# Kernel tuning notes

Hardware: AMD Instinct MI355X
Metric: run time of the kernel (lower is better)

Reference implementation:

```python
import jax, jax.numpy as jnp
import numpy as np

B, T, HW, N, HID, K, OUT = 8, 64, 64, 64, 64, 2, 1
DT = 0.1


def setup_inputs() -> dict:
    key = jax.random.key(0)
    ks = jax.random.split(key, 16)
    nrm = lambda k, shape, s: jax.random.normal(k, shape, jnp.float32) * s
    return {
        "frames": jax.random.uniform(ks[0], (B, T, HW, HW, 3), jnp.float32),
        "adjacency": jax.random.uniform(ks[1], (B, T, N, N), jnp.float32) / N,
        "hidden0": jnp.zeros((B, N, HID), jnp.float32),
        "Wc1": nrm(ks[2], (32, 3, 3, 3), 0.3), "bc1": jnp.zeros(32, jnp.float32),
        "Wc2": nrm(ks[3], (64, 32, 3, 3), 0.08), "bc2": jnp.zeros(64, jnp.float32),
        "Wc3": nrm(ks[4], (128, 64, 3, 3), 0.06), "bc3": jnp.zeros(128, jnp.float32),
        "We": nrm(ks[5], (128, HID), 0.09), "be": jnp.zeros(HID, jnp.float32),
        "Wh": nrm(ks[6], (K + 1, HID, HID), 0.12),
        "Wx": nrm(ks[7], (K + 1, HID, HID), 0.12),
        "bg": jnp.zeros(HID, jnp.float32),
        "tau": jnp.ones(HID, jnp.float32),
        "Ap": nrm(ks[8], (HID,), 1.0),
        "Wd1": nrm(ks[9], (HID, 128), 0.12), "bd1": jnp.zeros(128, jnp.float32),
        "Wd2": nrm(ks[10], (128, 64), 0.09), "bd2": jnp.zeros(64, jnp.float32),
        "Wd3": nrm(ks[11], (64, OUT), 0.12), "bd3": jnp.zeros(OUT, jnp.float32),
    }


def _conv_relu(x, w, b, stride):
    # torch Conv2d(k=3, stride=2, padding=1) == explicit padding (1,1)
    y = jax.lax.conv_general_dilated(
        x, w, (stride, stride), [(1, 1), (1, 1)],
        dimension_numbers=("NCHW", "OIHW", "NCHW"))
    return jax.nn.relu(y + b[None, :, None, None])


def _forward(frames, adjacency, hidden0, Wc1, bc1, Wc2, bc2, Wc3, bc3,
             We, be, Wh, Wx, bg, tau, Ap, Wd1, bd1, Wd2, bd2, Wd3, bd3):
    Bn, Tn, Hh, Ww, C = frames.shape
    # faithful to torch .view(-1, C, H, W): raw memory reinterpretation
    x = frames.reshape(Bn * Tn, C, Hh, Ww)
    x = _conv_relu(x, Wc1, bc1, 2)   # [BT,32,32,32]
    x = _conv_relu(x, Wc2, bc2, 2)   # [BT,64,16,16]
    x = _conv_relu(x, Wc3, bc3, 2)   # [BT,128,8,8]; AdaptiveAvgPool2d((8,8)) is identity here
    feats = x.reshape(Bn, Tn, 128, 8, 8).transpose(0, 1, 3, 4, 2).reshape(Bn, Tn, 64, 128)
    node = feats @ We + be           # [B,T,N,HID]

    Kp = Wh.shape[0] - 1
    eye = jnp.eye(adjacency.shape[-1], dtype=frames.dtype)

    def step(h, inputs):
        xt, At = inputs              # [B,N,HID], [B,N,N]
        powers = [jnp.broadcast_to(eye, At.shape)]
        p = At
        for _ in range(Kp):          # static K-loop -> [I, A, ..., A^K]
            powers.append(p)
            p = jnp.matmul(p, At)
        S = jnp.stack(powers)        # [K+1,B,N,N]
        z = jnp.einsum("bnd,kde->kbne", h, Wh) + jnp.einsum("bnd,kde->kbne", xt, Wx)
        gc = jnp.einsum("kbnm,kbme->bne", S, z) + bg
        f = jnp.tanh(gc)
        h_next = h + DT * (-(1.0 / tau + f) * h + f * Ap)  # liquid time-constant Euler step
        m = h_next.mean(axis=1)      # [B,HID]
        d = jax.nn.relu(m @ Wd1 + bd1)
        d = jax.nn.relu(d @ Wd2 + bd2)
        c = d @ Wd3 + bd3            # [B,OUT]
        return h_next, c

    xs = (node.transpose(1, 0, 2, 3), adjacency.transpose(1, 0, 2, 3))
    final_h, controls = jax.lax.scan(step, hidden0, xs)
    controls = controls.transpose(1, 0, 2)  # [B,T,OUT]
    return controls, final_h


def reference(frames, adjacency, hidden0, Wc1, bc1, Wc2, bc2, Wc3, bc3,
              We, be, Wh, Wx, bg, tau, Ap, Wd1, bd1, Wd2, bd2, Wd3, bd3):
    return _forward(frames, adjacency, hidden0, Wc1, bc1, Wc2, bc2, Wc3, bc3,
                    We, be, Wh, Wx, bg, tau, Ap, Wd1, bd1, Wd2, bd2, Wd3, bd3)
```

## Files before the change

kernel.cpp:

```cpp
#include <hip/hip_runtime.h>
#include <hip/hip_bf16.h>

#define SH 68
#define DT_C 0.1f

typedef short bfrag __attribute__((ext_vector_type(8)));
typedef _Float16 hfrag __attribute__((ext_vector_type(8)));
typedef float f32x4 __attribute__((ext_vector_type(4)));

union FU { bfrag v; unsigned short s[8]; uint4 q; };
union HU { hfrag v; unsigned short s[8]; uint4 q; };

__device__ __forceinline__ unsigned short bf16_rn(float x) {
  union { float f; unsigned u; } v; v.f = x;
  unsigned r = v.u + 0x7fffu + ((v.u >> 16) & 1u);
  return (unsigned short)(r >> 16);
}
__device__ __forceinline__ float bf16_tof(unsigned short h) {
  union { unsigned u; float f; } v; v.u = ((unsigned)h) << 16; return v.f;
}
__device__ __forceinline__ unsigned short bfu(float x) {
  union { __hip_bfloat16 b; unsigned short u; } cv;
  cv.b = __float2bfloat16(x);
  return cv.u;
}
__device__ __forceinline__ float tanh_f(float x) {
  return 1.0f - 2.0f / (__expf(2.0f * x) + 1.0f);
}
__device__ __forceinline__ void h16split(float v, unsigned short& hu, unsigned short& lu) {
  union { _Float16 h; unsigned short u; } a, b;
  a.h = (_Float16)v;
  b.h = (_Float16)(v - (float)a.h);
  hu = a.u; lu = b.u;
}
__device__ __forceinline__ unsigned short h16hi(float v) {
  union { _Float16 h; unsigned short u; } a; a.h = (_Float16)v; return a.u;
}

__device__ __forceinline__ void mm16(const float* __restrict__ A,
                                     const float* __restrict__ B, int sb,
                                     float acc[4][4], int n0, int e0) {
  #pragma unroll 4
  for (int k4 = 0; k4 < 16; ++k4) {
    float4 av0 = *(const float4*)(A + (n0+0)*SH + k4*4);
    float4 av1 = *(const float4*)(A + (n0+1)*SH + k4*4);
    float4 av2 = *(const float4*)(A + (n0+2)*SH + k4*4);
    float4 av3 = *(const float4*)(A + (n0+3)*SH + k4*4);
    const float a0j[4] = {av0.x, av0.y, av0.z, av0.w};
    const float a1j[4] = {av1.x, av1.y, av1.z, av1.w};
    const float a2j[4] = {av2.x, av2.y, av2.z, av2.w};
    const float a3j[4] = {av3.x, av3.y, av3.z, av3.w};
    #pragma unroll
    for (int j = 0; j < 4; ++j) {
      const float4 bv = *(const float4*)(B + (k4*4+j)*sb + e0);
      acc[0][0]+=a0j[j]*bv.x; acc[0][1]+=a0j[j]*bv.y; acc[0][2]+=a0j[j]*bv.z; acc[0][3]+=a0j[j]*bv.w;
      acc[1][0]+=a1j[j]*bv.x; acc[1][1]+=a1j[j]*bv.y; acc[1][2]+=a1j[j]*bv.z; acc[1][3]+=a1j[j]*bv.w;
      acc[2][0]+=a2j[j]*bv.x; acc[2][1]+=a2j[j]*bv.y; acc[2][2]+=a2j[j]*bv.z; acc[2][3]+=a2j[j]*bv.w;
      acc[3][0]+=a3j[j]*bv.x; acc[3][1]+=a3j[j]*bv.y; acc[3][2]+=a3j[j]*bv.z; acc[3][3]+=a3j[j]*bv.w;
    }
  }
}

__global__ __launch_bounds__(256) void wprep_k(const float* __restrict__ Wc2,
                                               const float* __restrict__ Wc3,
                                               const float* __restrict__ Wh,
                                               unsigned short* __restrict__ W2h,
                                               unsigned short* __restrict__ W2l,
                                               unsigned short* __restrict__ W3h,
                                               unsigned short* __restrict__ W3l,
                                               unsigned short* __restrict__ WTh,
                                               unsigned short* __restrict__ WTl) {
  int i = blockIdx.x * 256 + threadIdx.x;
  if (i < 18432) {
    int oc = i / 288, rem = i % 288, pos = rem >> 5, ic = rem & 31;
    float v = Wc2[oc*288 + ic*9 + pos];
    h16split(v, W2h[i], W2l[i]);
  } else if (i < 18432 + 73728) {
    int j = i - 18432;
    int oc = j / 576, rem = j % 576, pos = rem >> 6, ic = rem & 63;
    float v = Wc3[oc*576 + ic*9 + pos];
    h16split(v, W3h[j], W3l[j]);
  } else if (i < 18432 + 73728 + 12288) {
    int j = i - 92160;
    int k3 = j >> 12, rem = j & 4095, din = rem >> 6, dout = rem & 63;
    float v = Wh[j];
    unsigned short hi = bf16_rn(v);
    WTh[k3*4096 + dout*64 + din] = hi;
    WTl[k3*4096 + dout*64 + din] = bf16_rn(v - bf16_tof(hi));
  }
}

__global__ __launch_bounds__(256) void conv1_k(const float* __restrict__ frames,
                                               const float* __restrict__ W,
                                               const float* __restrict__ bias,
                                               unsigned short* __restrict__ c1h) {
  __shared__ __align__(16) float sIn[12288];
  int bt = blockIdx.x, tid = threadIdx.x;
  const float4* src = (const float4*)(frames + (size_t)bt * 12288);
  for (int i = tid; i < 3072; i += 256) ((float4*)sIn)[i] = src[i];
  __syncthreads();
  for (int p = tid; p < 1024; p += 256) {
    int ho = p >> 5, wo = p & 31, hi0 = ho*2-1, wi0 = wo*2-1;
    int obase = (((ho*2 + (wo&1))*16 + (wo>>1)))*8;
    for (int ocb = 0; ocb < 4; ++ocb) {
      float acc[8];
      #pragma unroll
      for (int j = 0; j < 8; ++j) acc[j] = bias[ocb*8+j];
      for (int ic = 0; ic < 3; ++ic) {
        float win[9];
        #pragma unroll
        for (int kh = 0; kh < 3; ++kh) {
          int hi = hi0 + kh;
          #pragma unroll
          for (int kw = 0; kw < 3; ++kw) {
            int wi = wi0 + kw;
            win[kh*3+kw] = (hi>=0 && hi<64 && wi>=0 && wi<64) ? sIn[ic*4096 + hi*64 + wi] : 0.f;
          }
        }
        #pragma unroll
        for (int j = 0; j < 8; ++j) {
          const float* wp = W + (size_t)(ocb*8+j)*27 + ic*9;
          #pragma unroll
          for (int k = 0; k < 9; ++k) acc[j] += win[k] * wp[k];
        }
      }
      ushort hh[8];
      #pragma unroll
      for (int j = 0; j < 8; ++j) hh[j] = h16hi(fmaxf(acc[j], 0.f));
      *(uint4*)&c1h[(size_t)bt*32768 + ocb*8192 + obase] = *(uint4*)hh;
    }
  }
}

#define MFMAH(a, bb, cc) __builtin_amdgcn_mfma_f32_16x16x32_f16((a), (bb), (cc), 0, 0, 0)

__global__ __launch_bounds__(256) void conv2m_k(const unsigned short* __restrict__ c1h,
                                                const unsigned short* __restrict__ W2h,
                                                const unsigned short* __restrict__ W2l,
                                                const float* __restrict__ bias,
                                                unsigned short* __restrict__ c2h) {
  __shared__ __align__(16) unsigned short sH[32768];
  int bt = blockIdx.x, tid = threadIdx.x;
  {
    const uint4* gh = (const uint4*)(c1h + (size_t)bt*32768);
    for (int i = tid; i < 4096; i += 256) ((uint4*)sH)[i] = gh[i];
  }
  __syncthreads();
  int lane = tid & 63, w = tid >> 6, g = lane >> 4, c = lane & 15;
  f32x4 acc[4][4] = {};
  const uint4 z4 = make_uint4(0,0,0,0);
  #pragma unroll
  for (int pos = 0; pos < 9; ++pos) {
    const int kh = pos / 3, kw = pos % 3;
    HU Ah[4];
    #pragma unroll
    for (int m = 0; m < 4; ++m) {
      int pix = w*64 + m*16 + c;
      int ho = pix >> 4, wo = pix & 15;
      int hi = 2*ho - 1 + kh, wi = 2*wo - 1 + kw;
      bool ok = (hi >= 0) & (wi >= 0);
      int hic = ok ? hi : 0, wic = ok ? wi : 0;
      int a = (((g*32 + hic)*2 + (wic & 1))*16 + (wic >> 1))*8;
      uint4 vh = *(const uint4*)&sH[a];
      Ah[m].q = ok ? vh : z4;
    }
    HU Bh[4], Bl[4];
    #pragma unroll
    for (int n = 0; n < 4; ++n) {
      int off = (n*16 + c)*288 + pos*32 + g*8;
      Bh[n].q = *(const uint4*)(W2h + off);
      Bl[n].q = *(const uint4*)(W2l + off);
    }
    #pragma unroll
    for (int m = 0; m < 4; ++m)
      #pragma unroll
      for (int n = 0; n < 4; ++n) {
        acc[m][n] = MFMAH(Ah[m].v, Bh[n].v, acc[m][n]);
        acc[m][n] = MFMAH(Ah[m].v, Bl[n].v, acc[m][n]);
      }
  }
  #pragma unroll
  for (int n = 0; n < 4; ++n) {
    int oc = n*16 + c;
    float bv = bias[oc];
    int ks3 = oc >> 3, il = oc & 7;
    #pragma unroll
    for (int m = 0; m < 4; ++m) {
      #pragma unroll
      for (int r = 0; r < 4; ++r) {
        int pix = w*64 + m*16 + 4*g + r;
        int ho = pix >> 4, wo = pix & 15;
        float v = fmaxf(acc[m][n][r] + bv, 0.f);
        size_t dst = (size_t)bt*16384 + ((((ks3*16 + ho)*2 + (wo&1))*8 + (wo>>1)))*8 + il;
        c2h[dst] = h16hi(v);
      }
    }
  }
}

__global__ __launch_bounds__(256) void conv3m_k(const unsigned short* __restrict__ c2h,
                                                const unsigned short* __restrict__ W3h,
                                                const unsigned short* __restrict__ W3l,
                                                const float* __restrict__ bias,
                                                float* __restrict__ c3) {
  __shared__ __align__(16) unsigned short sH[16384];
  int bt = blockIdx.x, tid = threadIdx.x;
  {
    const uint4* gh = (const uint4*)(c2h + (size_t)bt*16384);
    for (int i = tid; i < 2048; i += 256) ((uint4*)sH)[i] = gh[i];
  }
  __syncthreads();
  int lane = tid & 63, w = tid >> 6, g = lane >> 4, c = lane & 15;
  f32x4 acc[8] = {};
  const uint4 z4 = make_uint4(0,0,0,0);
  int pix = w*16 + c;
  int ho = pix >> 3, wo = pix & 7;
  #pragma unroll
  for (int pos = 0; pos < 9; ++pos) {
    const int kh = pos / 3, kw = pos % 3;
    int hi = 2*ho - 1 + kh, wi = 2*wo - 1 + kw;
    bool ok = (hi >= 0) & (wi >= 0);
    int hic = ok ? hi : 0, wic = ok ? wi : 0;
    #pragma unroll
    for (int ih = 0; ih < 2; ++ih) {
      int icg = ih*4 + g;
      int a = ((((icg*16 + hic)*2 + (wic & 1))*8 + (wic >> 1)))*8;
      HU Ah;
      uint4 vh = *(const uint4*)&sH[a];
      Ah.q = ok ? vh : z4;
      #pragma unroll
      for (int n = 0; n < 8; ++n) {
        int off = (n*16 + c)*576 + pos*64 + ih*32 + g*8;
        HU Bh, Bl;
        Bh.q = *(const uint4*)(W3h + off);
        Bl.q = *(const uint4*)(W3l + off);
        acc[n] = MFMAH(Ah.v, Bh.v, acc[n]);
        acc[n] = MFMAH(Ah.v, Bl.v, acc[n]);
      }
    }
  }
  #pragma unroll
  for (int n = 0; n < 8; ++n) {
    int oc = n*16 + c;
    float bv = bias[oc];
    #pragma unroll
    for (int r = 0; r < 4; ++r) {
      int po = w*16 + 4*g + r;
      c3[(size_t)(bt*128 + oc)*64 + po] = fmaxf(acc[n][r] + bv, 0.f);
    }
  }
}

__global__ __launch_bounds__(256) void embed_k(const float* __restrict__ c3,
                                               const float* __restrict__ We,
                                               const float* __restrict__ be,
                                               float* __restrict__ node) {
  __shared__ float sF[64*133];
  __shared__ __align__(16) float sWe[8192];
  int bt = blockIdx.x, tid = threadIdx.x;
  const float* src = c3 + (size_t)bt * 8192;
  for (int i = tid; i < 8192; i += 256) sF[(i & 63)*133 + (i >> 6)] = src[i];
  const float4* w4 = (const float4*)We;
  for (int i = tid; i < 2048; i += 256) ((float4*)sWe)[i] = w4[i];
  __syncthreads();
  int lane = tid & 63, w = tid >> 6, nsub = lane >> 4, eb = lane & 15;
  int n0 = w*16 + nsub*4, e0 = eb*4;
  float acc[4][4];
  #pragma unroll
  for (int jj = 0; jj < 4; ++jj)
    #pragma unroll
    for (int ee = 0; ee < 4; ++ee) acc[jj][ee] = be[e0+ee];
  for (int c = 0; c < 128; ++c) {
    float a0 = sF[(n0+0)*133+c];
    float a1 = sF[(n0+1)*133+c];
    float a2 = sF[(n0+2)*133+c];
    float a3 = sF[(n0+3)*133+c];
    const float4 bv = *(const float4*)&sWe[c*64 + e0];
    acc[0][0]+=a0*bv.x; acc[0][1]+=a0*bv.y; acc[0][2]+=a0*bv.z; acc[0][3]+=a0*bv.w;
    acc[1][0]+=a1*bv.x; acc[1][1]+=a1*bv.y; acc[1][2]+=a1*bv.z; acc[1][3]+=a1*bv.w;
    acc[2][0]+=a2*bv.x; acc[2][1]+=a2*bv.y; acc[2][2]+=a2*bv.z; acc[2][3]+=a2*bv.w;
    acc[3][0]+=a3*bv.x; acc[3][1]+=a3*bv.y; acc[3][2]+=a3*bv.z; acc[3][3]+=a3*bv.w;
  }
  float4* nd = (float4*)(node + (size_t)bt * 4096);
  #pragma unroll
  for (int jj = 0; jj < 4; ++jj)
    nd[(n0+jj)*16 + eb] = make_float4(acc[jj][0], acc[jj][1], acc[jj][2], acc[jj][3]);
}

__global__ __launch_bounds__(256) void prep_k(const float* __restrict__ adj,
                                              const float* __restrict__ node,
                                              const float* __restrict__ Wx,
                                              unsigned short* __restrict__ Abf,
                                              unsigned short* __restrict__ A2bf,
                                              float* __restrict__ gxg) {
  __shared__ __align__(16) float sA[64*SH], sA2[64*SH], sN[64*SH], sZ[64*SH];
  int bt = blockIdx.x, tid = threadIdx.x;
  {
    const float4* a4 = (const float4*)(adj + (size_t)bt * 4096);
    const float4* n4 = (const float4*)(node + (size_t)bt * 4096);
    for (int i = tid; i < 1024; i += 256) {
      int r = i >> 4, c = (i & 15) * 4;
      *(float4*)&sA[r*SH+c] = a4[i];
      *(float4*)&sN[r*SH+c] = n4[i];
    }
  }
  __syncthreads();
  int lane = tid & 63, w = tid >> 6, nsub = lane >> 4, eb = lane & 15;
  int n0 = w*16 + nsub*4, e0 = eb*4;
  float4* gxout = (float4*)(gxg + (size_t)bt * 4096);
  for (int i = tid; i < 1024; i += 256) {
    int r = i >> 4, c0 = (i & 15) * 4;
    ushort4 o;
    o.x = bf16_rn(sA[r*SH+c0+0]); o.y = bf16_rn(sA[r*SH+c0+1]);
    o.z = bf16_rn(sA[r*SH+c0+2]); o.w = bf16_rn(sA[r*SH+c0+3]);
    *(ushort4*)&Abf[(size_t)bt*4096 + r*64 + c0] = o;
  }
  {
    float a2t[4][4] = {};
    mm16(sA, sA, SH, a2t, n0, e0);
    #pragma unroll
    for (int jj = 0; jj < 4; ++jj) {
      *(float4*)&sA2[(n0+jj)*SH+e0] = make_float4(a2t[jj][0], a2t[jj][1], a2t[jj][2], a2t[jj][3]);
      ushort4 o;
      o.x = bf16_rn(a2t[jj][0]); o.y = bf16_rn(a2t[jj][1]);
      o.z = bf16_rn(a2t[jj][2]); o.w = bf16_rn(a2t[jj][3]);
      *(ushort4*)&A2bf[(size_t)bt*4096 + (n0+jj)*64 + e0] = o;
    }
  }
  {
    float t[4][4] = {};
    mm16(sN, Wx + 4096, 64, t, n0, e0);
    #pragma unroll
    for (int jj = 0; jj < 4; ++jj)
      *(float4*)&sZ[(n0+jj)*SH+e0] = make_float4(t[jj][0], t[jj][1], t[jj][2], t[jj][3]);
  }
  __syncthreads();
  float gx[4][4] = {};
  mm16(sA, sZ, SH, gx, n0, e0);
  __syncthreads();
  {
    float t[4][4] = {};
    mm16(sN, Wx + 8192, 64, t, n0, e0);
    #pragma unroll
    for (int jj = 0; jj < 4; ++jj)
      *(float4*)&sZ[(n0+jj)*SH+e0] = make_float4(t[jj][0], t[jj][1], t[jj][2], t[jj][3]);
  }
  __syncthreads();
  mm16(sA2, sZ, SH, gx, n0, e0);
  mm16(sN, Wx, 64, gx, n0, e0);
  #pragma unroll
  for (int jj = 0; jj < 4; ++jj)
    gxout[(n0+jj)*16 + eb] = make_float4(gx[jj][0], gx[jj][1], gx[jj][2], gx[jj][3]);
}

#define MFMA(a, bb, cc) __builtin_amdgcn_mfma_f32_16x16x32_bf16((a), (bb), (cc), 0, 0, 0)

__global__ __launch_bounds__(1024, 4) void seq2_k(
    const unsigned short* __restrict__ Abf, const unsigned short* __restrict__ A2bf,
    const float* __restrict__ gxg, const float* __restrict__ h0,
    const unsigned short* __restrict__ WTh, const unsigned short* __restrict__ WTl,
    const float* __restrict__ bg, const float* __restrict__ tau, const float* __restrict__ Apv,
    float* __restrict__ mout, float* __restrict__ out) {
  __shared__ unsigned short sHh[64*72];
  __shared__ unsigned short sA[2][64*72], sA2[2][64*72];
  __shared__ unsigned short sZ1[64*72], sZ2[64*72];
  __shared__ float sPart[64*17];
  int b = blockIdx.x, tid = threadIdx.x;
  int lane = tid & 63, w = tid >> 6, g = lane >> 4, c = lane & 15;
  int mt = w & 3, nt = w >> 2;
  int e = nt*16 + c;
  int mrow = mt*16 + 4*g;
  float itau = 1.f/tau[e], apv = Apv[e], bgv = bg[e];
  FU wf[3][2][2];
  #pragma unroll
  for (int k3 = 0; k3 < 3; ++k3)
    #pragma unroll
    for (int kt = 0; kt < 2; ++kt) {
      int off = k3*4096 + e*64 + kt*32 + 8*g;
      wf[k3][kt][0].q = *(const uint4*)(WTh + off);
      wf[k3][kt][1].q = *(const uint4*)(WTl + off);
    }
  float hm[4];
  #pragma unroll
  for (int r = 0; r < 4; ++r) hm[r] = h0[(size_t)b*4096 + (mrow+r)*64 + e];
  #pragma unroll
  for (int r = 0; r < 4; ++r) sHh[(mrow+r)*72 + e] = bfu(hm[r]);
  {
    int row = tid >> 4, k0 = (tid & 15) * 4;
    *(uint2*)&sA[0][row*72 + k0]  = *(const uint2*)(Abf  + (size_t)b*64*4096 + tid*4);
    *(uint2*)&sA2[0][row*72 + k0] = *(const uint2*)(A2bf + (size_t)b*64*4096 + tid*4);
  }
  __syncthreads();
  #pragma unroll 1
  for (int t = 0; t < 64; ++t) {
    int cur = t & 1;
    size_t bt = (size_t)b*64 + t;
    int tn = (t < 63) ? t + 1 : t;
    uint2 pa  = *(const uint2*)(Abf  + ((size_t)b*64 + tn)*4096 + tid*4);
    uint2 pa2 = *(const uint2*)(A2bf + ((size_t)b*64 + tn)*4096 + tid*4);
    float gxv[4];
    {
      const float* gp = gxg + bt*4096;
      #pragma unroll
      for (int r = 0; r < 4; ++r) gxv[r] = gp[(mrow+r)*64 + e];
    }
    FU ha[2];
    #pragma unroll
    for (int kt = 0; kt < 2; ++kt)
      ha[kt].q = *(const uint4*)&sHh[(mt*16 + c)*72 + kt*32 + 8*g];
    f32x4 a1a = {0.f,0.f,0.f,0.f}, a1b = {0.f,0.f,0.f,0.f};
    f32x4 a2a = {0.f,0.f,0.f,0.f}, a2b = {0.f,0.f,0.f,0.f};
    a1a = MFMA(ha[0].v, wf[1][0][0].v, a1a);
    a1a = MFMA(ha[0].v, wf[1][0][1].v, a1a);
    a1b = MFMA(ha[1].v, wf[1][1][0].v, a1b);
    a1b = MFMA(ha[1].v, wf[1][1][1].v, a1b);
    a2a = MFMA(ha[0].v, wf[2][0][0].v, a2a);
    a2a = MFMA(ha[0].v, wf[2][0][1].v, a2a);
    a2b = MFMA(ha[1].v, wf[2][1][0].v, a2b);
    a2b = MFMA(ha[1].v, wf[2][1][1].v, a2b);
    f32x4 a1 = a1a + a1b, a2 = a2a + a2b;
    {
      ushort4 o1, o2;
      o1.x = bfu(a1[0]); o1.y = bfu(a1[1]); o1.z = bfu(a1[2]); o1.w = bfu(a1[3]);
      o2.x = bfu(a2[0]); o2.y = bfu(a2[1]); o2.z = bfu(a2[2]); o2.w = bfu(a2[3]);
      *(ushort4*)&sZ1[e*72 + mrow] = o1;
      *(ushort4*)&sZ2[e*72 + mrow] = o2;
    }
    __syncthreads();
    f32x4 acc0 = {0.f,0.f,0.f,0.f}, acc1 = {0.f,0.f,0.f,0.f};
    #pragma unroll
    for (int kt = 0; kt < 2; ++kt) {
      FU aA, aA2, z1f, z2f;
      int ao = (mt*16 + c)*72 + kt*32 + 8*g;
      aA.q  = *(const uint4*)&sA[cur][ao];
      aA2.q = *(const uint4*)&sA2[cur][ao];
      z1f.q = *(const uint4*)&sZ1[e*72 + kt*32 + 8*g];
      z2f.q = *(const uint4*)&sZ2[e*72 + kt*32 + 8*g];
      f32x4& acc = kt ? acc1 : acc0;
      acc = MFMA(ha[kt].v, wf[0][kt][0].v, acc);
      acc = MFMA(ha[kt].v, wf[0][kt][1].v, acc);
      acc = MFMA(aA.v,  z1f.v, acc);
      acc = MFMA(aA2.v, z2f.v, acc);
    }
    f32x4 acc = acc0 + acc1;
    float ps = 0.f;
    #pragma unroll
    for (int r = 0; r < 4; ++r) {
      float gc = acc[r] + gxv[r] + bgv;
      float f = tanh_f(gc);
      float hn = hm[r] + DT_C * (-(itau + f) * hm[r] + f * apv);
      hm[r] = hn;
      ps += hn;
      sHh[(mrow+r)*72 + e] = bfu(hn);
    }
    sPart[e*17 + mt*4 + g] = ps;
    {
      int row = tid >> 4, k0 = (tid & 15) * 4;
      *(uint2*)&sA[cur^1][row*72 + k0]  = pa;
      *(uint2*)&sA2[cur^1][row*72 + k0] = pa2;
    }
    __syncthreads();
    if (lane < 4) {
      int ee = w*4 + lane;
      float s = 0.f;
      #pragma unroll
      for (int j = 0; j < 16; ++j) s += sPart[ee*17 + j];
      mout[bt*64 + ee] = s * (1.0f / 64.0f);
    }
  }
  #pragma unroll
  for (int r = 0; r < 4; ++r)
    out[512 + (size_t)b*4096 + (mrow+r)*64 + e] = hm[r];
}

__global__ __launch_bounds__(128) void dec_k(const float* __restrict__ mout,
                                             const float* __restrict__ Wd1, const float* __restrict__ bd1,
                                             const float* __restrict__ Wd2, const float* __restrict__ bd2,
                                             const float* __restrict__ Wd3, const float* __restrict__ bd3,
                                             float* __restrict__ out) {
  __shared__ float sm[64], sd1[128], sd2[64];
  int bt = blockIdx.x, tid = threadIdx.x;
  if (tid < 64) sm[tid] = mout[(size_t)bt*64 + tid];
  __syncthreads();
  {
    float a = bd1[tid];
    #pragma unroll 8
    for (int e = 0; e < 64; ++e) a += sm[e] * Wd1[e*128 + tid];
    sd1[tid] = fmaxf(a, 0.f);
  }
  __syncthreads();
  if (tid < 64) {
    float a = bd2[tid];
    #pragma unroll 8
    for (int i = 0; i < 128; ++i) a += sd1[i] * Wd2[i*64 + tid];
    sd2[tid] = fmaxf(a, 0.f);
  }
  __syncthreads();
  if (tid < 64) {
    float p = sd2[tid] * Wd3[tid];
    #pragma unroll
    for (int off = 32; off > 0; off >>= 1) p += __shfl_down(p, off, 64);
    if (tid == 0) out[bt] = p + bd3[0];
  }
}

extern "C" void kernel_launch(void* const* d_in, const int* in_sizes, int n_in,
                              void* d_out, int out_size, void* d_ws, size_t ws_size,
                              hipStream_t stream) {
  const float* frames = (const float*)d_in[0];
  const float* adj    = (const float*)d_in[1];
  const float* h0     = (const float*)d_in[2];
  const float* Wc1 = (const float*)d_in[3];  const float* bc1 = (const float*)d_in[4];
  const float* Wc2 = (const float*)d_in[5];  const float* bc2 = (const float*)d_in[6];
  const float* Wc3 = (const float*)d_in[7];  const float* bc3 = (const float*)d_in[8];
  const float* We  = (const float*)d_in[9];  const float* be  = (const float*)d_in[10];
  const float* Wh  = (const float*)d_in[11]; const float* Wx  = (const float*)d_in[12];
  const float* bg  = (const float*)d_in[13]; const float* tau = (const float*)d_in[14];
  const float* Ap  = (const float*)d_in[15];
  const float* Wd1 = (const float*)d_in[16]; const float* bd1 = (const float*)d_in[17];
  const float* Wd2 = (const float*)d_in[18]; const float* bd2 = (const float*)d_in[19];
  const float* Wd3 = (const float*)d_in[20]; const float* bd3 = (const float*)d_in[21];

  float* ws = (float*)d_ws;
  unsigned short* c1h = (unsigned short*)(ws);
  unsigned short* c2h = (unsigned short*)(ws + 16777216);
  unsigned short* W2h = (unsigned short*)(ws + 20971520);
  unsigned short* W2l = (unsigned short*)(ws + 20980736);
  unsigned short* W3h = (unsigned short*)(ws + 20989952);
  unsigned short* W3l = (unsigned short*)(ws + 21026816);
  unsigned short* WTh = (unsigned short*)(ws + 21063680);
  unsigned short* WTl = (unsigned short*)(ws + 21069824);
  float* c3   = ws;
  float* node = ws + 4194304;
  float* gx   = ws + 6291456;
  unsigned short* Abf  = (unsigned short*)(ws + 8388608);
  unsigned short* A2bf = (unsigned short*)(ws + 9437184);
  float* mo   = ws + 10485760;
  float* out  = (float*)d_out;

  wprep_k <<<408, 256, 0, stream>>>(Wc2, Wc3, Wh, W2h, W2l, W3h, W3l, WTh, WTl);
  conv1_k <<<512, 256, 0, stream>>>(frames, Wc1, bc1, c1h);
  conv2m_k<<<512, 256, 0, stream>>>(c1h, W2h, W2l, bc2, c2h);
  conv3m_k<<<512, 256, 0, stream>>>(c2h, W3h, W3l, bc3, c3);
  embed_k <<<512, 256, 0, stream>>>(c3, We, be, node);
  prep_k  <<<512, 256, 0, stream>>>(adj, node, Wx, Abf, A2bf, gx);
  seq2_k  <<<8,  1024, 0, stream>>>(Abf, A2bf, gx, h0, WTh, WTl, bg, tau, Ap, mo, out);
  dec_k   <<<512, 128, 0, stream>>>(mo, Wd1, bd1, Wd2, bd2, Wd3, bd3, out);
}
```

Measured before the change: 320.2 us.

## Fuse node embedding into conv3 with fp16 MFMA; simplify seq accumulators

Fuses the embedding projection into the conv3 kernel. The conv3 output stays in shared memory as fp16 and is multiplied by a pre-transposed, hi/lo-split We using MFMA, so the fp32 c3 round trip through global memory and a separate kernel launch go away. The weight-prep kernel gains a section that transposes and splits We. The recurrent kernel also merges its paired partial accumulators into single chains, which shortens code but lengthens the MFMA dependency chains on the serial critical path. Rounding conv3 activations to fp16 before the embedding may slightly change accuracy.

```diff
diff --git a/kernel.cpp b/kernel.cpp
--- a/kernel.cpp
+++ b/kernel.cpp
@@ -64,12 +64,15 @@
 __global__ __launch_bounds__(256) void wprep_k(const float* __restrict__ Wc2,
                                                const float* __restrict__ Wc3,
                                                const float* __restrict__ Wh,
+                                               const float* __restrict__ We,
                                                unsigned short* __restrict__ W2h,
                                                unsigned short* __restrict__ W2l,
                                                unsigned short* __restrict__ W3h,
                                                unsigned short* __restrict__ W3l,
                                                unsigned short* __restrict__ WTh,
-                                               unsigned short* __restrict__ WTl) {
+                                               unsigned short* __restrict__ WTl,
+                                               unsigned short* __restrict__ WeTh,
+                                               unsigned short* __restrict__ WeTl) {
   int i = blockIdx.x * 256 + threadIdx.x;
   if (i < 18432) {
     int oc = i / 288, rem = i % 288, pos = rem >> 5, ic = rem & 31;
@@ -87,6 +90,11 @@
     unsigned short hi = bf16_rn(v);
     WTh[k3*4096 + dout*64 + din] = hi;
     WTl[k3*4096 + dout*64 + din] = bf16_rn(v - bf16_tof(hi));
+  } else if (i < 18432 + 73728 + 12288 + 8192) {
+    int j = i - 104448;
+    int e = j >> 7, oc = j & 127;
+    float v = We[oc*64 + e];
+    h16split(v, WeTh[j], WeTl[j]);
   }
 }
 
@@ -198,12 +206,16 @@
   }
 }
 
-__global__ __launch_bounds__(256) void conv3m_k(const unsigned short* __restrict__ c2h,
+__global__ __launch_bounds__(256) void conv3e_k(const unsigned short* __restrict__ c2h,
                                                 const unsigned short* __restrict__ W3h,
                                                 const unsigned short* __restrict__ W3l,
                                                 const float* __restrict__ bias,
-                                                float* __restrict__ c3) {
+                                                const unsigned short* __restrict__ WeTh,
+                                                const unsigned short* __restrict__ WeTl,
+                                                const float* __restrict__ be,
+                                                float* __restrict__ node) {
   __shared__ __align__(16) unsigned short sH[16384];
+  __shared__ __align__(16) unsigned short sF[64*136];
   int bt = blockIdx.x, tid = threadIdx.x;
   {
     const uint4* gh = (const uint4*)(c2h + (size_t)bt*16384);
@@ -246,45 +258,35 @@
     #pragma unroll
     for (int r = 0; r < 4; ++r) {
       int po = w*16 + 4*g + r;
-      c3[(size_t)(bt*128 + oc)*64 + po] = fmaxf(acc[n][r] + bv, 0.f);
-    }
-  }
-}
-
-__global__ __launch_bounds__(256) void embed_k(const float* __restrict__ c3,
-                                               const float* __restrict__ We,
-                                               const float* __restrict__ be,
-                                               float* __restrict__ node) {
-  __shared__ float sF[64*133];
-  __shared__ __align__(16) float sWe[8192];
-  int bt = blockIdx.x, tid = threadIdx.x;
-  const float* src = c3 + (size_t)bt * 8192;
-  for (int i = tid; i < 8192; i += 256) sF[(i & 63)*133 + (i >> 6)] = src[i];
-  const float4* w4 = (const float4*)We;
-  for (int i = tid; i < 2048; i += 256) ((float4*)sWe)[i] = w4[i];
-  __syncthreads();
-  int lane = tid & 63, w = tid >> 6, nsub = lane >> 4, eb = lane & 15;
-  int n0 = w*16 + nsub*4, e0 = eb*4;
-  float acc[4][4];
-  #pragma unroll
-  for (int jj = 0; jj < 4; ++jj)
-    #pragma unroll
-    for (int ee = 0; ee < 4; ++ee) acc[jj][ee] = be[e0+ee];
-  for (int c = 0; c < 128; ++c) {
-    float a0 = sF[(n0+0)*133+c];
-    float a1 = sF[(n0+1)*133+c];
-    float a2 = sF[(n0+2)*133+c];
-    float a3 = sF[(n0+3)*133+c];
-    const float4 bv = *(const float4*)&sWe[c*64 + e0];
-    acc[0][0]+=a0*bv.x; acc[0][1]+=a0*bv.y; acc[0][2]+=a0*bv.z; acc[0][3]+=a0*bv.w;
-    acc[1][0]+=a1*bv.x; acc[1][1]+=a1*bv.y; acc[1][2]+=a1*bv.z; acc[1][3]+=a1*bv.w;
-    acc[2][0]+=a2*bv.x; acc[2][1]+=a2*bv.y; acc[2][2]+=a2*bv.z; acc[2][3]+=a2*bv.w;
-    acc[3][0]+=a3*bv.x; acc[3][1]+=a3*bv.y; acc[3][2]+=a3*bv.z; acc[3][3]+=a3*bv.w;
-  }
-  float4* nd = (float4*)(node + (size_t)bt * 4096);
-  #pragma unroll
-  for (int jj = 0; jj < 4; ++jj)
-    nd[(n0+jj)*16 + eb] = make_float4(acc[jj][0], acc[jj][1], acc[jj][2], acc[jj][3]);
+      sF[po*136 + oc] = h16hi(fmaxf(acc[n][r] + bv, 0.f));
+    }
+  }
+  __syncthreads();
+  f32x4 eacc[4] = {{0.f,0.f,0.f,0.f},{0.f,0.f,0.f,0.f},{0.f,0.f,0.f,0.f},{0.f,0.f,0.f,0.f}};
+  #pragma unroll
+  for (int kt = 0; kt < 4; ++kt) {
+    HU Af;
+    Af.q = *(const uint4*)&sF[(w*16 + c)*136 + kt*32 + g*8];
+    #pragma unroll
+    for (int n = 0; n < 4; ++n) {
+      int off = (n*16 + c)*128 + kt*32 + g*8;
+      HU Bh, Bl;
+      Bh.q = *(const uint4*)(WeTh + off);
+      Bl.q = *(const uint4*)(WeTl + off);
+      eacc[n] = MFMAH(Af.v, Bh.v, eacc[n]);
+      eacc[n] = MFMAH(Af.v, Bl.v, eacc[n]);
+    }
+  }
+  #pragma unroll
+  for (int n = 0; n < 4; ++n) {
+    int e = n*16 + c;
+    float bev = be[e];
+    #pragma unroll
+    for (int r = 0; r < 4; ++r) {
+      int po = w*16 + 4*g + r;
+      node[(size_t)bt*4096 + po*64 + e] = eacc[n][r] + bev;
+    }
+  }
 }
 
 __global__ __launch_bounds__(256) void prep_k(const float* __restrict__ adj,
@@ -408,17 +410,14 @@
     #pragma unroll
     for (int kt = 0; kt < 2; ++kt)
       ha[kt].q = *(const uint4*)&sHh[(mt*16 + c)*72 + kt*32 + 8*g];
-    f32x4 a1a = {0.f,0.f,0.f,0.f}, a1b = {0.f,0.f,0.f,0.f};
-    f32x4 a2a = {0.f,0.f,0.f,0.f}, a2b = {0.f,0.f,0.f,0.f};
-    a1a = MFMA(ha[0].v, wf[1][0][0].v, a1a);
-    a1a = MFMA(ha[0].v, wf[1][0][1].v, a1a);
-    a1b = MFMA(ha[1].v, wf[1][1][0].v, a1b);
-    a1b = MFMA(ha[1].v, wf[1][1][1].v, a1b);
-    a2a = MFMA(ha[0].v, wf[2][0][0].v, a2a);
-    a2a = MFMA(ha[0].v, wf[2][0][1].v, a2a);
-    a2b = MFMA(ha[1].v, wf[2][1][0].v, a2b);
-    a2b = MFMA(ha[1].v, wf[2][1][1].v, a2b);
-    f32x4 a1 = a1a + a1b, a2 = a2a + a2b;
+    f32x4 a1 = {0.f,0.f,0.f,0.f}, a2 = {0.f,0.f,0.f,0.f};
+    #pragma unroll
+    for (int kt = 0; kt < 2; ++kt) {
+      a1 = MFMA(ha[kt].v, wf[1][kt][0].v, a1);
+      a1 = MFMA(ha[kt].v, wf[1][kt][1].v, a1);
+      a2 = MFMA(ha[kt].v, wf[2][kt][0].v, a2);
+      a2 = MFMA(ha[kt].v, wf[2][kt][1].v, a2);
+    }
     {
       ushort4 o1, o2;
       o1.x = bfu(a1[0]); o1.y = bfu(a1[1]); o1.z = bfu(a1[2]); o1.w = bfu(a1[3]);
@@ -427,7 +426,7 @@
       *(ushort4*)&sZ2[e*72 + mrow] = o2;
     }
     __syncthreads();
-    f32x4 acc0 = {0.f,0.f,0.f,0.f}, acc1 = {0.f,0.f,0.f,0.f};
+    f32x4 acc = {0.f,0.f,0.f,0.f};
     #pragma unroll
     for (int kt = 0; kt < 2; ++kt) {
       FU aA, aA2, z1f, z2f;
@@ -436,13 +435,11 @@
       aA2.q = *(const uint4*)&sA2[cur][ao];
       z1f.q = *(const uint4*)&sZ1[e*72 + kt*32 + 8*g];
       z2f.q = *(const uint4*)&sZ2[e*72 + kt*32 + 8*g];
-      f32x4& acc = kt ? acc1 : acc0;
       acc = MFMA(ha[kt].v, wf[0][kt][0].v, acc);
       acc = MFMA(ha[kt].v, wf[0][kt][1].v, acc);
       acc = MFMA(aA.v,  z1f.v, acc);
       acc = MFMA(aA2.v, z2f.v, acc);
     }
-    f32x4 acc = acc0 + acc1;
     float ps = 0.f;
     #pragma unroll
     for (int r = 0; r < 4; ++r) {
@@ -530,7 +527,8 @@
   unsigned short* W3l = (unsigned short*)(ws + 21026816);
   unsigned short* WTh = (unsigned short*)(ws + 21063680);
   unsigned short* WTl = (unsigned short*)(ws + 21069824);
-  float* c3   = ws;
+  unsigned short* WeTh = (unsigned short*)(ws + 21075968);
+  unsigned short* WeTl = (unsigned short*)(ws + 21080064);
   float* node = ws + 4194304;
   float* gx   = ws + 6291456;
   unsigned short* Abf  = (unsigned short*)(ws + 8388608);
@@ -538,11 +536,10 @@
   float* mo   = ws + 10485760;
   float* out  = (float*)d_out;
 
-  wprep_k <<<408, 256, 0, stream>>>(Wc2, Wc3, Wh, W2h, W2l, W3h, W3l, WTh, WTl);
+  wprep_k <<<440, 256, 0, stream>>>(Wc2, Wc3, Wh, We, W2h, W2l, W3h, W3l, WTh, WTl, WeTh, WeTl);
   conv1_k <<<512, 256, 0, stream>>>(frames, Wc1, bc1, c1h);
   conv2m_k<<<512, 256, 0, stream>>>(c1h, W2h, W2l, bc2, c2h);
-  conv3m_k<<<512, 256, 0, stream>>>(c2h, W3h, W3l, bc3, c3);
-  embed_k <<<512, 256, 0, stream>>>(c3, We, be, node);
+  conv3e_k<<<512, 256, 0, stream>>>(c2h, W3h, W3l, bc3, WeTh, WeTl, be, node);
   prep_k  <<<512, 256, 0, stream>>>(adj, node, Wx, Abf, A2bf, gx);
   seq2_k  <<<8,  1024, 0, stream>>>(Abf, A2bf, gx, h0, WTh, WTl, bg, tau, Ap, mo, out);
   dec_k   <<<512, 128, 0, stream>>>(mo, Wd1, bd1, Wd2, bd2, Wd3, bd3, out);
```

Result: faster. 302.2 us (-5.6%).
